# Kernel optimization log

Hardware: AMD Instinct MI355X
Metric: run time of the kernel (lower is better)

The kernel has to match this reference:

```python
import jax, jax.numpy as jnp
import numpy as np

B, S, V, H = 64, 512, 128, 1024
TEMP = 1.0


def _lstm_layer(x_seq, W_ih, W_hh, b_ih, b_hh):
    """x_seq: (S, B, D_in) -> (S, B, H). PyTorch gate order: i, f, g, o."""
    Hh = W_hh.shape[1]
    Bb = x_seq.shape[1]
    # precompute input projections for all timesteps: (S, B, 4H)
    xW = jnp.einsum('sbd,gd->sbg', x_seq, W_ih) + (b_ih + b_hh)

    def step(carry, xw_t):
        h, c = carry
        gates = xw_t + h @ W_hh.T  # (B, 4H)
        i, f, g, o = jnp.split(gates, 4, axis=-1)
        i = jax.nn.sigmoid(i)
        f = jax.nn.sigmoid(f)
        g = jnp.tanh(g)
        o = jax.nn.sigmoid(o)
        c = f * c + i * g
        h = o * jnp.tanh(c)
        return (h, c), h

    h0 = jnp.zeros((Bb, Hh), dtype=x_seq.dtype)
    c0 = jnp.zeros((Bb, Hh), dtype=x_seq.dtype)
    _, hs = jax.lax.scan(step, (h0, c0), xW)
    return hs  # (S, B, H)


def setup_inputs() -> dict:
    key = jax.random.key(0)
    ks = jax.random.split(key, 11)
    s = 1.0 / np.sqrt(H)
    u = lambda k, shape: jax.random.uniform(k, shape, jnp.float32, -s, s)
    return {
        'x': jax.random.normal(ks[0], (B, S, V), jnp.float32),
        'W_ih0': u(ks[1], (4 * H, V)),
        'W_hh0': u(ks[2], (4 * H, H)),
        'b_ih0': u(ks[3], (4 * H,)),
        'b_hh0': u(ks[4], (4 * H,)),
        'W_ih1': u(ks[5], (4 * H, H)),
        'W_hh1': u(ks[6], (4 * H, H)),
        'b_ih1': u(ks[7], (4 * H,)),
        'b_hh1': u(ks[8], (4 * H,)),
        'W_fc': u(ks[9], (V, H)),
        'b_fc': u(ks[10], (V,)),
    }


def reference(x, W_ih0, W_hh0, b_ih0, b_hh0, W_ih1, W_hh1, b_ih1, b_hh1, W_fc, b_fc):
    xs = jnp.transpose(x, (1, 0, 2))  # (S, B, V)
    h1 = _lstm_layer(xs, W_ih0, W_hh0, b_ih0, b_hh0)   # (S, B, H)
    h2 = _lstm_layer(h1, W_ih1, W_hh1, b_ih1, b_hh1)   # (S, B, H)
    logits = jnp.einsum('sbh,vh->sbv', h2, W_fc) + b_fc  # (S, B, V)
    out = jax.nn.log_softmax(logits * TEMP, axis=-1)
    return jnp.transpose(out, (1, 0, 2))  # (B, S, V)
```

## Files before the change

### kernel.cpp

```cpp
#include <hip/hip_runtime.h>
#include <hip/hip_bf16.h>
#include <math.h>


#define S_LEN 512
#define B_SZ  64
#define V_SZ  128
#define H_SZ  1024
#define BH    65536
#define RING  32
#define SLOT  66560
#define FSTR  16
#define INVP  20

typedef unsigned short u16;
typedef unsigned short u16x8 __attribute__((ext_vector_type(8)));
typedef __bf16         bf16x8 __attribute__((ext_vector_type(8)));
typedef float          f32x4  __attribute__((ext_vector_type(4)));
typedef int            i32x4  __attribute__((ext_vector_type(4)));

__device__ __forceinline__ u16 f2bf(float f) {
    unsigned int u = __float_as_uint(f);
    u += 0x7fffu + ((u >> 16) & 1u);
    return (u16)(u >> 16);
}
__device__ __forceinline__ f32x4 mfma16(u16x8 a, u16x8 b, f32x4 c) {
    return __builtin_amdgcn_mfma_f32_16x16x32_bf16(
        __builtin_bit_cast(bf16x8, a), __builtin_bit_cast(bf16x8, b), c, 0, 0, 0);
}
__device__ __forceinline__ f32x4 mfma16(i32x4 a, u16x8 b, f32x4 c) {
    return __builtin_amdgcn_mfma_f32_16x16x32_bf16(
        __builtin_bit_cast(bf16x8, a), __builtin_bit_cast(bf16x8, b), c, 0, 0, 0);
}

__device__ __forceinline__ void ld_g(i32x4& d, const u16* p) {
    asm volatile("global_load_dwordx4 %0, %1, off" : "=v"(d) : "v"(p));
}
__device__ __forceinline__ void st_coh16(u16* p, u16x8 v) {
    i32x4 vv = __builtin_bit_cast(i32x4, v);
    asm volatile("global_store_dwordx4 %0, %1, off sc0 sc1" :: "v"(p), "v"(vv));
}
__device__ __forceinline__ int ld_flag(const int* p) {
    int v;
    asm volatile("global_load_dword %0, %1, off sc0 sc1\n\ts_waitcnt vmcnt(0)"
                 : "=v"(v) : "v"(p) : "memory");
    return v;
}
__device__ __forceinline__ void st_flag(int* p, int v) {
    asm volatile("global_store_dword %0, %1, off sc0 sc1" :: "v"(p), "v"(v));
}
#define WAITV(n) asm volatile("s_waitcnt vmcnt(" #n ")" ::: "memory")
#define LGKM0    asm volatile("s_waitcnt lgkmcnt(0)" ::: "memory")
#define SCHEDB   __builtin_amdgcn_sched_barrier(0)

__device__ __forceinline__ void l2_acquire_inv() {
    __builtin_amdgcn_fence(__ATOMIC_ACQUIRE, "agent");
}

__global__ __launch_bounds__(256) void cvt_kernel(const float* __restrict__ s,
                                                  u16* __restrict__ d, int n)
{
    int i = (blockIdx.x * 256 + threadIdx.x) * 4;
    if (i >= n) return;
    float4 v = *(const float4*)(s + i);
    ushort4 o;
    o.x = f2bf(v.x); o.y = f2bf(v.y); o.z = f2bf(v.z); o.w = f2bf(v.w);
    *(ushort4*)(d + i) = o;
}

union SMemL {
    struct { u16 whh[64 * 1024]; u16 wih[64 * 128]; u16 tr[4][384]; } l0;
    struct { u16 w[64 * 1024]; u16 tr[4][384]; } l1;
    float lg[16][132];
};

__global__ __launch_bounds__(256, 1) void persist_kernel(
    const u16* __restrict__ xb,
    const u16* __restrict__ Wih0c, const u16* __restrict__ Whh0c,
    const u16* __restrict__ Wih1c, const u16* __restrict__ Whh1c,
    const u16* __restrict__ Wfcc,
    const float* __restrict__ bih0, const float* __restrict__ bhh0,
    const float* __restrict__ bih1, const float* __restrict__ bhh1,
    const float* __restrict__ bfc,
    u16* __restrict__ h0b, u16* __restrict__ h1b,
    int* __restrict__ flagL0, int* __restrict__ flagL1, int* __restrict__ flagFC,
    float* __restrict__ out)
{
    __shared__ SMemL sm;
    const int bid = blockIdx.x, tid = threadIdx.x;
    const int wave = tid >> 6, lane = tid & 63;
    const int l16 = lane & 15, kgi = lane >> 4, kg8 = kgi * 8;

    if (bid < 64) {
        const int j0 = bid * 16, jj = j0 + l16;
        for (int ch = tid; ch < 1024; ch += 256) {
            int row = ch >> 4, kc = ch & 15;
            int gr = (row >> 4) * H_SZ + j0 + (row & 15);
            int bo = (row * 256 + kc * 16) ^ ((row & 7) << 4);
            *(u16x8*)((char*)sm.l0.wih + bo) = *(const u16x8*)(Wih0c + (size_t)gr * V_SZ + kc * 8);
        }
        for (int ch = tid; ch < 8192; ch += 256) {
            int row = ch >> 7, kc = ch & 127;
            int gr = (row >> 4) * H_SZ + j0 + (row & 15);
            int bo = (row * 2048 + kc * 16) ^ ((row & 7) << 4);
            *(u16x8*)((char*)sm.l0.whh + bo) = *(const u16x8*)(Whh0c + (size_t)gr * H_SZ + kc * 8);
        }
        __syncthreads();

        const float bii = bih0[jj]            + bhh0[jj];
        const float bif = bih0[H_SZ + jj]     + bhh0[H_SZ + jj];
        const float big = bih0[2 * H_SZ + jj] + bhh0[2 * H_SZ + jj];
        const float bio = bih0[3 * H_SZ + jj] + bhh0[3 * H_SZ + jj];

        const int swz = (l16 & 7) << 4;
        int whh_rb[4], wih_rb[4];
        #pragma unroll
        for (int g = 0; g < 4; ++g) {
            whh_rb[g] = (g * 16 + l16) * 2048 + kgi * 16;
            wih_rb[g] = (g * 16 + l16) * 256 + kgi * 16;
        }
        const int arow = wave * 16 + l16;
        const u16* xrow = xb + (size_t)arow * (S_LEN * V_SZ);
        u16* trw = sm.l0.tr[wave];
        float creg[4] = {0.f, 0.f, 0.f, 0.f};

        for (int t = 0; t < S_LEN; ++t) {
            i32x4 xq[4];
            {
                const u16* xp = xrow + (size_t)t * V_SZ + kg8;
                #pragma unroll
                for (int i = 0; i < 4; ++i) ld_g(xq[i], xp + i * 32);
            }
            {
                const int* p = nullptr; int tgt = 0;
                if (tid < 64)                      { p = flagL0 + tid * FSTR;        tgt = t; }
                else if (tid < 192 && t >= RING)   { p = flagL1 + (tid - 64) * FSTR; tgt = t - (RING - 1); }
                if (p && tgt > 0) while (ld_flag(p) < tgt) __builtin_amdgcn_s_sleep(2);
                __syncthreads();
            }
            if (t >= INVP && (t % INVP) == 0) l2_acquire_inv();
            WAITV(0); SCHEDB;

            f32x4 acc[4][2] = {};
            auto ISSUE = [&](i32x4 (&buf)[8], const u16* base) {
                #pragma unroll
                for (int q = 0; q < 8; ++q) ld_g(buf[q], base + q * 32);
            };
            auto COMP = [&](i32x4 (&buf)[8], int k0) {
                #pragma unroll
                for (int q = 0; q < 8; ++q)
                    #pragma unroll
                    for (int g = 0; g < 4; ++g)
                        acc[g][q & 1] = mfma16(buf[q],
                            *(const u16x8*)((char*)sm.l0.whh + ((whh_rb[g] + (k0 + q) * 64) ^ swz)),
                            acc[g][q & 1]);
            };
            const u16* aB = h0b + (size_t)((t - 1) & (RING - 1)) * SLOT
                          + (size_t)arow * H_SZ + kg8;
            i32x4 b0[8], b1[8], b2[8];
            ISSUE(b0, aB); ISSUE(b1, aB + 256); ISSUE(b2, aB + 512);
            SCHEDB;
            #pragma unroll
            for (int i = 0; i < 4; ++i)
                #pragma unroll
                for (int g = 0; g < 4; ++g)
                    acc[g][i & 1] = mfma16(xq[i],
                        *(const u16x8*)((char*)sm.l0.wih + ((wih_rb[g] + i * 64) ^ swz)),
                        acc[g][i & 1]);
            WAITV(16); SCHEDB; COMP(b0, 0);  ISSUE(b0, aB + 768);
            WAITV(16); SCHEDB; COMP(b1, 8);
            WAITV(8);  SCHEDB; COMP(b2, 16);
            WAITV(0);  SCHEDB; COMP(b0, 24);

            {
                u16* hout = h0b + (size_t)(t & (RING - 1)) * SLOT;
                #pragma unroll
                for (int r = 0; r < 4; ++r) {
                    const float ip = acc[0][0][r] + acc[0][1][r] + bii;
                    const float fp = acc[1][0][r] + acc[1][1][r] + bif;
                    const float gp = acc[2][0][r] + acc[2][1][r] + big;
                    const float op = acc[3][0][r] + acc[3][1][r] + bio;
                    const float iv = 1.f / (1.f + expf(-ip));
                    const float fv = 1.f / (1.f + expf(-fp));
                    const float gv = tanhf(gp);
                    const float ov = 1.f / (1.f + expf(-op));
                    const float cv = fv * creg[r] + iv * gv;
                    creg[r] = cv;
                    trw[(kgi * 4 + r) * 24 + l16] = f2bf(ov * tanhf(cv));
                }
                LGKM0; SCHEDB;
                if (lane < 32) {
                    int m = lane >> 1, jb = lane & 1;
                    u16x8 v = *(const u16x8*)&trw[m * 24 + jb * 8];
                    st_coh16(hout + (size_t)(wave * 16 + m) * H_SZ + j0 + jb * 8, v);
                }
                WAITV(0);
            }
            __syncthreads();
            if (tid == 0) st_flag(flagL0 + bid * FSTR, t + 1);
        }
        return;
    }

    if (bid < 192) {
        const int lb = bid - 64, j0 = lb * 8, jj2 = j0 + (l16 & 7);
        for (int ch = tid; ch < 8192; ch += 256) {
            int ldsrow = ch >> 7, kc = ch & 127;
            int region = ldsrow >> 5, rl = ldsrow & 31;
            int gr = (rl >> 3) * H_SZ + j0 + (rl & 7);
            const u16* src = (region ? Whh1c : Wih1c) + (size_t)gr * H_SZ + kc * 8;
            int bo = (ldsrow * 2048 + kc * 16) ^ ((ldsrow & 7) << 4);
            *(u16x8*)((char*)sm.l1.w + bo) = *(const u16x8*)src;
        }
        __syncthreads();

        const float bii = bih1[jj2]            + bhh1[jj2];
        const float bif = bih1[H_SZ + jj2]     + bhh1[H_SZ + jj2];
        const float big = bih1[2 * H_SZ + jj2] + bhh1[2 * H_SZ + jj2];
        const float bio = bih1[3 * H_SZ + jj2] + bhh1[3 * H_SZ + jj2];
        const bool lo = (l16 < 8);

        const int swz = (l16 & 7) << 4;
        int wrb[2][2];
        #pragma unroll
        for (int region = 0; region < 2; ++region)
            #pragma unroll
            for (int nt = 0; nt < 2; ++nt)
                wrb[region][nt] = (region * 32 + nt * 16 + l16) * 2048 + kgi * 16;
        const int arow = wave * 16 + l16;
        u16* trw = sm.l1.tr[wave];
        float creg[4] = {0.f, 0.f, 0.f, 0.f};

        for (int t = 0; t < S_LEN; ++t) {
            {
                const int* p = nullptr; int tgt = 0;
                if (tid < 64)                        { p = flagL0 + tid * FSTR;         tgt = t + 1; }
                else if (tid < 192)                  { p = flagL1 + (tid - 64) * FSTR;  tgt = t; }
                else if (tid < 196 && t >= RING)     { p = flagFC + (tid - 192) * FSTR; tgt = t - (RING - 1); }
                if (p && tgt > 0) while (ld_flag(p) < tgt) __builtin_amdgcn_s_sleep(2);
                __syncthreads();
            }
            if (t >= INVP && (t % INVP) == 0) l2_acquire_inv();

            f32x4 acc[2][2] = {};
            auto ISSUE = [&](i32x4 (&buf)[8], const u16* base) {
                #pragma unroll
                for (int q = 0; q < 8; ++q) ld_g(buf[q], base + q * 32);
            };
            auto COMP = [&](i32x4 (&buf)[8], int region, int k0) {
                #pragma unroll
                for (int q = 0; q < 8; ++q)
                    #pragma unroll
                    for (int nt = 0; nt < 2; ++nt)
                        acc[nt][q & 1] = mfma16(buf[q],
                            *(const u16x8*)((char*)sm.l1.w + ((wrb[region][nt] + (k0 + q) * 64) ^ swz)),
                            acc[nt][q & 1]);
            };
            const u16* a1 = h0b + (size_t)(t & (RING - 1)) * SLOT + (size_t)arow * H_SZ + kg8;
            const u16* a2 = h1b + (size_t)((t - 1) & (RING - 1)) * SLOT + (size_t)arow * H_SZ + kg8;
            i32x4 b0[8], b1[8], b2[8];
            ISSUE(b0, a1); ISSUE(b1, a1 + 256); ISSUE(b2, a1 + 512);
            SCHEDB;
            WAITV(16); SCHEDB; COMP(b0, 0, 0);  ISSUE(b0, a1 + 768);
            WAITV(16); SCHEDB; COMP(b1, 0, 8);  ISSUE(b1, a2);
            WAITV(16); SCHEDB; COMP(b2, 0, 16); ISSUE(b2, a2 + 256);
            WAITV(16); SCHEDB; COMP(b0, 0, 24); ISSUE(b0, a2 + 512);
            WAITV(16); SCHEDB; COMP(b1, 1, 0);  ISSUE(b1, a2 + 768);
            WAITV(16); SCHEDB; COMP(b2, 1, 8);
            WAITV(8);  SCHEDB; COMP(b0, 1, 16);
            WAITV(0);  SCHEDB; COMP(b1, 1, 24);

            {
                #pragma unroll
                for (int r = 0; r < 4; ++r) {
                    const float s0 = acc[0][0][r] + acc[0][1][r];
                    const float s1 = acc[1][0][r] + acc[1][1][r];
                    const float q0 = __shfl_xor(s0, 8);
                    const float q1 = __shfl_xor(s1, 8);
                    const float ip = (lo ? s0 : q0) + bii;
                    const float fp = (lo ? q0 : s0) + bif;
                    const float gp = (lo ? s1 : q1) + big;
                    const float op = (lo ? q1 : s1) + bio;
                    const float iv = 1.f / (1.f + expf(-ip));
                    const float fv = 1.f / (1.f + expf(-fp));
                    const float gv = tanhf(gp);
                    const float ov = 1.f / (1.f + expf(-op));
                    const float cv = fv * creg[r] + iv * gv;
                    creg[r] = cv;
                    if (lo) trw[(kgi * 4 + r) * 24 + (l16 & 7)] = f2bf(ov * tanhf(cv));
                }
                LGKM0; SCHEDB;
                if (lane < 16) {
                    int m = lane;
                    u16x8 v = *(const u16x8*)&trw[m * 24];
                    st_coh16(h1b + (size_t)(t & (RING - 1)) * SLOT
                             + (size_t)(wave * 16 + m) * H_SZ + j0, v);
                }
                WAITV(0);
            }
            __syncthreads();
            if (tid == 0) st_flag(flagL1 + lb * FSTR, t + 1);
        }
        return;
    }

    {
        const int fb = bid - 192, m0 = fb * 16;
        const u16* wp[2];
        #pragma unroll
        for (int nt = 0; nt < 2; ++nt)
            wp[nt] = Wfcc + (size_t)(wave * 32 + nt * 16 + l16) * H_SZ + kg8;

        for (int t = 0; t < S_LEN; ++t) {
            {
                const int* p = nullptr; int tgt = 0;
                if (tid < 128) { p = flagL1 + tid * FSTR; tgt = t + 1; }
                if (p && tgt > 0) while (ld_flag(p) < tgt) __builtin_amdgcn_s_sleep(2);
                __syncthreads();
            }
            if (t >= INVP && (t % INVP) == 0) l2_acquire_inv();

            const u16* aB = h1b + (size_t)(t & (RING - 1)) * SLOT
                          + (size_t)(m0 + l16) * H_SZ + kg8;
            f32x4 acc[2][2] = {};
            i32x4 buf[8];
            WAITV(0);
            #pragma unroll
            for (int c = 0; c < 4; ++c) {
                #pragma unroll
                for (int q = 0; q < 8; ++q) ld_g(buf[q], aB + c * 256 + q * 32);
                WAITV(0); SCHEDB;
                #pragma unroll
                for (int q = 0; q < 8; ++q) {
                    #pragma unroll
                    for (int nt = 0; nt < 2; ++nt)
                        acc[nt][q & 1] = mfma16(buf[q],
                            *(const u16x8*)(wp[nt] + (c * 8 + q) * 32), acc[nt][q & 1]);
                }
            }
            #pragma unroll
            for (int nt = 0; nt < 2; ++nt)
                #pragma unroll
                for (int r = 0; r < 4; ++r) {
                    const int m = kgi * 4 + r, n = wave * 32 + nt * 16 + l16;
                    sm.lg[m][n] = acc[nt][0][r] + acc[nt][1][r] + bfc[n];
                }
            __syncthreads();
            const int row = tid >> 4, sub = tid & 15;
            float vals[8]; float mx = -1e30f;
            #pragma unroll
            for (int q = 0; q < 8; ++q) { vals[q] = sm.lg[row][sub * 8 + q]; mx = fmaxf(mx, vals[q]); }
            #pragma unroll
            for (int o = 1; o < 16; o <<= 1) mx = fmaxf(mx, __shfl_xor(mx, o));
            float se = 0.f;
            #pragma unroll
            for (int q = 0; q < 8; ++q) se += expf(vals[q] - mx);
            #pragma unroll
            for (int o = 1; o < 16; o <<= 1) se += __shfl_xor(se, o);
            const float ls = mx + logf(se);
            float* op = out + (size_t)(m0 + row) * (S_LEN * V_SZ) + (size_t)t * V_SZ + sub * 8;
            #pragma unroll
            for (int q = 0; q < 8; ++q) op[q] = vals[q] - ls;

            __syncthreads();
            if (tid == 0) st_flag(flagFC + fb * FSTR, t + 1);
        }
    }
}

extern "C" void kernel_launch(void* const* d_in, const int* in_sizes, int n_in,
                              void* d_out, int out_size, void* d_ws, size_t ws_size,
                              hipStream_t stream)
{
    const float* x    = (const float*)d_in[0];
    const float* Wih0 = (const float*)d_in[1];
    const float* Whh0 = (const float*)d_in[2];
    const float* bih0 = (const float*)d_in[3];
    const float* bhh0 = (const float*)d_in[4];
    const float* Wih1 = (const float*)d_in[5];
    const float* Whh1 = (const float*)d_in[6];
    const float* bih1 = (const float*)d_in[7];
    const float* bhh1 = (const float*)d_in[8];
    const float* Wfc  = (const float*)d_in[9];
    const float* bfc  = (const float*)d_in[10];
    float* out = (float*)d_out;

    u16* wih0 = (u16*)d_ws;
    u16* whh0 = wih0 + (size_t)4096 * 128;
    u16* wih1 = whh0 + (size_t)4096 * 1024;
    u16* whh1 = wih1 + (size_t)4096 * 1024;
    u16* wfc  = whh1 + (size_t)4096 * 1024;
    u16* xbuf = wfc  + (size_t)128 * 1024;
    u16* h0b  = xbuf + (size_t)B_SZ * S_LEN * V_SZ;
    u16* h1b  = h0b + (size_t)RING * SLOT;
    int* flags  = (int*)(h1b + (size_t)RING * SLOT);
    int* flagL0 = flags;
    int* flagL1 = flagL0 + 64 * FSTR;
    int* flagFC = flagL1 + 128 * FSTR;

    auto cvt = [&](const float* s, u16* d, int n) {
        cvt_kernel<<<(n / 4 + 255) / 256, 256, 0, stream>>>(s, d, n);
    };
    cvt(Wih0, wih0, 4096 * 128);
    cvt(Whh0, whh0, 4096 * 1024);
    cvt(Wih1, wih1, 4096 * 1024);
    cvt(Whh1, whh1, 4096 * 1024);
    cvt(Wfc,  wfc,  128 * 1024);
    cvt(x,    xbuf, B_SZ * S_LEN * V_SZ);
    hipMemsetAsync(h0b + (size_t)(RING - 1) * SLOT, 0, (size_t)BH * sizeof(u16), stream);
    hipMemsetAsync(h1b + (size_t)(RING - 1) * SLOT, 0, (size_t)BH * sizeof(u16), stream);
    hipMemsetAsync(flags, 0, (size_t)196 * FSTR * sizeof(int), stream);

    persist_kernel<<<196, 256, 0, stream>>>(
        xbuf, wih0, whh0, wih1, whh1, wfc,
        bih0, bhh0, bih1, bhh1, bfc,
        h0b, h1b, flagL0, flagL1, flagFC, out);
}
```

Before: 6.385 ms.

## Split layer-1 flag wait to overlap h0 GEMM, pad LDS rows instead of XOR swizzle

Layer-1 blocks now wait only on the layer-0 flag before starting the W_ih1·h0 half of the matmul. The layer-1 recurrent flag is polled asynchronously mid-computation and checked just before loading h1, so the wait on the slowest layer-1 block overlaps useful MFMA work. Flag polls use an async load with a single fast-path check before falling into the spin loop. Weight LDS tiles switch from XOR swizzle to padded row strides (1040/144), which simplifies addressing but uses more shared memory and adds an extra __syncthreads per step.

```diff
diff --git a/kernel.cpp b/kernel.cpp
--- a/kernel.cpp
+++ b/kernel.cpp
@@ -12,6 +12,7 @@
 #define SLOT  66560
 #define FSTR  16
 #define INVP  20
+#define WSTR  1040
 
 typedef unsigned short u16;
 typedef unsigned short u16x8 __attribute__((ext_vector_type(8)));
@@ -45,6 +46,12 @@
     asm volatile("global_load_dword %0, %1, off sc0 sc1\n\ts_waitcnt vmcnt(0)"
                  : "=v"(v) : "v"(p) : "memory");
     return v;
+}
+__device__ __forceinline__ void ld_flag_async(int& v, const int* p) {
+    asm volatile("global_load_dword %0, %1, off sc0 sc1" : "=v"(v) : "v"(p));
+}
+__device__ __forceinline__ void flag_fence(int& v) {
+    asm volatile("s_waitcnt vmcnt(0)" : "+v"(v) :: "memory");
 }
 __device__ __forceinline__ void st_flag(int* p, int v) {
     asm volatile("global_store_dword %0, %1, off sc0 sc1" :: "v"(p), "v"(v));
@@ -69,8 +76,8 @@
 }
 
 union SMemL {
-    struct { u16 whh[64 * 1024]; u16 wih[64 * 128]; u16 tr[4][384]; } l0;
-    struct { u16 w[64 * 1024]; u16 tr[4][384]; } l1;
+    struct { u16 whh[64 * WSTR]; u16 wih[64 * 144]; u16 tr[4][384]; } l0;
+    struct { u16 w[64 * WSTR]; u16 tr[4][384]; } l1;
     float lg[16][132];
 };
 
@@ -96,14 +103,14 @@
         for (int ch = tid; ch < 1024; ch += 256) {
             int row = ch >> 4, kc = ch & 15;
             int gr = (row >> 4) * H_SZ + j0 + (row & 15);
-            int bo = (row * 256 + kc * 16) ^ ((row & 7) << 4);
-            *(u16x8*)((char*)sm.l0.wih + bo) = *(const u16x8*)(Wih0c + (size_t)gr * V_SZ + kc * 8);
+            *(u16x8*)&sm.l0.wih[row * 144 + kc * 8] =
+                *(const u16x8*)(Wih0c + (size_t)gr * V_SZ + kc * 8);
         }
         for (int ch = tid; ch < 8192; ch += 256) {
             int row = ch >> 7, kc = ch & 127;
             int gr = (row >> 4) * H_SZ + j0 + (row & 15);
-            int bo = (row * 2048 + kc * 16) ^ ((row & 7) << 4);
-            *(u16x8*)((char*)sm.l0.whh + bo) = *(const u16x8*)(Whh0c + (size_t)gr * H_SZ + kc * 8);
+            *(u16x8*)&sm.l0.whh[row * WSTR + kc * 8] =
+                *(const u16x8*)(Whh0c + (size_t)gr * H_SZ + kc * 8);
         }
         __syncthreads();
 
@@ -112,12 +119,11 @@
         const float big = bih0[2 * H_SZ + jj] + bhh0[2 * H_SZ + jj];
         const float bio = bih0[3 * H_SZ + jj] + bhh0[3 * H_SZ + jj];
 
-        const int swz = (l16 & 7) << 4;
-        int whh_rb[4], wih_rb[4];
+        int whh_b[4], wih_b[4];
         #pragma unroll
         for (int g = 0; g < 4; ++g) {
-            whh_rb[g] = (g * 16 + l16) * 2048 + kgi * 16;
-            wih_rb[g] = (g * 16 + l16) * 256 + kgi * 16;
+            whh_b[g] = (g * 16 + l16) * WSTR + kg8;
+            wih_b[g] = (g * 16 + l16) * 144 + kg8;
         }
         const int arow = wave * 16 + l16;
         const u16* xrow = xb + (size_t)arow * (S_LEN * V_SZ);
@@ -131,15 +137,15 @@
                 #pragma unroll
                 for (int i = 0; i < 4; ++i) ld_g(xq[i], xp + i * 32);
             }
-            {
-                const int* p = nullptr; int tgt = 0;
-                if (tid < 64)                      { p = flagL0 + tid * FSTR;        tgt = t; }
-                else if (tid < 192 && t >= RING)   { p = flagL1 + (tid - 64) * FSTR; tgt = t - (RING - 1); }
-                if (p && tgt > 0) while (ld_flag(p) < tgt) __builtin_amdgcn_s_sleep(2);
-                __syncthreads();
-            }
+            const int* pA = nullptr; int tgtA = 0; int fvA = 0x7fffffff;
+            if (tid < 64)                    { pA = flagL0 + tid * FSTR;        tgtA = t; }
+            else if (tid < 192 && t >= RING) { pA = flagL1 + (tid - 64) * FSTR; tgtA = t - (RING - 1); }
+            if (pA && tgtA > 0) ld_flag_async(fvA, pA);
+            flag_fence(fvA);
+            if (pA && tgtA > 0 && fvA < tgtA)
+                while (ld_flag(pA) < tgtA) __builtin_amdgcn_s_sleep(2);
+            __syncthreads();
             if (t >= INVP && (t % INVP) == 0) l2_acquire_inv();
-            WAITV(0); SCHEDB;
 
             f32x4 acc[4][2] = {};
             auto ISSUE = [&](i32x4 (&buf)[8], const u16* base) {
@@ -152,7 +158,7 @@
                     #pragma unroll
                     for (int g = 0; g < 4; ++g)
                         acc[g][q & 1] = mfma16(buf[q],
-                            *(const u16x8*)((char*)sm.l0.whh + ((whh_rb[g] + (k0 + q) * 64) ^ swz)),
+                            *(const u16x8*)&sm.l0.whh[whh_b[g] + (k0 + q) * 32],
                             acc[g][q & 1]);
             };
             const u16* aB = h0b + (size_t)((t - 1) & (RING - 1)) * SLOT
@@ -165,8 +171,7 @@
                 #pragma unroll
                 for (int g = 0; g < 4; ++g)
                     acc[g][i & 1] = mfma16(xq[i],
-                        *(const u16x8*)((char*)sm.l0.wih + ((wih_rb[g] + i * 64) ^ swz)),
-                        acc[g][i & 1]);
+                        *(const u16x8*)&sm.l0.wih[wih_b[g] + i * 32], acc[g][i & 1]);
             WAITV(16); SCHEDB; COMP(b0, 0);  ISSUE(b0, aB + 768);
             WAITV(16); SCHEDB; COMP(b1, 8);
             WAITV(8);  SCHEDB; COMP(b2, 16);
@@ -209,8 +214,7 @@
             int region = ldsrow >> 5, rl = ldsrow & 31;
             int gr = (rl >> 3) * H_SZ + j0 + (rl & 7);
             const u16* src = (region ? Whh1c : Wih1c) + (size_t)gr * H_SZ + kc * 8;
-            int bo = (ldsrow * 2048 + kc * 16) ^ ((ldsrow & 7) << 4);
-            *(u16x8*)((char*)sm.l1.w + bo) = *(const u16x8*)src;
+            *(u16x8*)&sm.l1.w[ldsrow * WSTR + kc * 8] = *(const u16x8*)src;
         }
         __syncthreads();
 
@@ -220,26 +224,27 @@
         const float bio = bih1[3 * H_SZ + jj2] + bhh1[3 * H_SZ + jj2];
         const bool lo = (l16 < 8);
 
-        const int swz = (l16 & 7) << 4;
         int wrb[2][2];
         #pragma unroll
         for (int region = 0; region < 2; ++region)
             #pragma unroll
             for (int nt = 0; nt < 2; ++nt)
-                wrb[region][nt] = (region * 32 + nt * 16 + l16) * 2048 + kgi * 16;
+                wrb[region][nt] = (region * 32 + nt * 16 + l16) * WSTR + kg8;
         const int arow = wave * 16 + l16;
         u16* trw = sm.l1.tr[wave];
         float creg[4] = {0.f, 0.f, 0.f, 0.f};
 
         for (int t = 0; t < S_LEN; ++t) {
-            {
-                const int* p = nullptr; int tgt = 0;
-                if (tid < 64)                        { p = flagL0 + tid * FSTR;         tgt = t + 1; }
-                else if (tid < 192)                  { p = flagL1 + (tid - 64) * FSTR;  tgt = t; }
-                else if (tid < 196 && t >= RING)     { p = flagFC + (tid - 192) * FSTR; tgt = t - (RING - 1); }
-                if (p && tgt > 0) while (ld_flag(p) < tgt) __builtin_amdgcn_s_sleep(2);
-                __syncthreads();
-            }
+            const int* pA = nullptr; int tgtA = 0; int fvA = 0x7fffffff;
+            if (tid < 64)                               { pA = flagL0 + tid * FSTR;         tgtA = t + 1; }
+            else if (tid >= 192 && tid < 196 && t >= RING) { pA = flagFC + (tid - 192) * FSTR; tgtA = t - (RING - 1); }
+            const int* pB = (tid < 128 && t > 0) ? (flagL1 + tid * FSTR) : nullptr;
+            int fvB = 0x7fffffff;
+            if (pA && tgtA > 0) ld_flag_async(fvA, pA);
+            flag_fence(fvA);
+            if (pA && tgtA > 0 && fvA < tgtA)
+                while (ld_flag(pA) < tgtA) __builtin_amdgcn_s_sleep(2);
+            __syncthreads();
             if (t >= INVP && (t % INVP) == 0) l2_acquire_inv();
 
             f32x4 acc[2][2] = {};
@@ -253,22 +258,27 @@
                     #pragma unroll
                     for (int nt = 0; nt < 2; ++nt)
                         acc[nt][q & 1] = mfma16(buf[q],
-                            *(const u16x8*)((char*)sm.l1.w + ((wrb[region][nt] + (k0 + q) * 64) ^ swz)),
+                            *(const u16x8*)&sm.l1.w[wrb[region][nt] + (k0 + q) * 32],
                             acc[nt][q & 1]);
             };
             const u16* a1 = h0b + (size_t)(t & (RING - 1)) * SLOT + (size_t)arow * H_SZ + kg8;
             const u16* a2 = h1b + (size_t)((t - 1) & (RING - 1)) * SLOT + (size_t)arow * H_SZ + kg8;
             i32x4 b0[8], b1[8], b2[8];
             ISSUE(b0, a1); ISSUE(b1, a1 + 256); ISSUE(b2, a1 + 512);
-            SCHEDB;
             WAITV(16); SCHEDB; COMP(b0, 0, 0);  ISSUE(b0, a1 + 768);
-            WAITV(16); SCHEDB; COMP(b1, 0, 8);  ISSUE(b1, a2);
-            WAITV(16); SCHEDB; COMP(b2, 0, 16); ISSUE(b2, a2 + 256);
-            WAITV(16); SCHEDB; COMP(b0, 0, 24); ISSUE(b0, a2 + 512);
-            WAITV(16); SCHEDB; COMP(b1, 1, 0);  ISSUE(b1, a2 + 768);
-            WAITV(16); SCHEDB; COMP(b2, 1, 8);
-            WAITV(8);  SCHEDB; COMP(b0, 1, 16);
-            WAITV(0);  SCHEDB; COMP(b1, 1, 24);
+            WAITV(16); SCHEDB; COMP(b1, 0, 8);
+            WAITV(8);  SCHEDB; COMP(b2, 0, 16);
+            if (pB) ld_flag_async(fvB, pB);
+            WAITV(0);  SCHEDB; COMP(b0, 0, 24);
+            flag_fence(fvB);
+            if (pB && fvB < t)
+                while (ld_flag(pB) < t) __builtin_amdgcn_s_sleep(2);
+            __syncthreads();
+            ISSUE(b0, a2); ISSUE(b1, a2 + 256); ISSUE(b2, a2 + 512);
+            WAITV(16); SCHEDB; COMP(b0, 1, 0);  ISSUE(b0, a2 + 768);
+            WAITV(16); SCHEDB; COMP(b1, 1, 8);
+            WAITV(8);  SCHEDB; COMP(b2, 1, 16);
+            WAITV(0);  SCHEDB; COMP(b0, 1, 24);
 
             {
                 #pragma unroll
@@ -313,9 +323,12 @@
 
         for (int t = 0; t < S_LEN; ++t) {
             {
-                const int* p = nullptr; int tgt = 0;
-                if (tid < 128) { p = flagL1 + tid * FSTR; tgt = t + 1; }
-                if (p && tgt > 0) while (ld_flag(p) < tgt) __builtin_amdgcn_s_sleep(2);
+                const int* pA = (tid < 128) ? (flagL1 + tid * FSTR) : nullptr;
+                int fvA = 0x7fffffff;
+                if (pA) ld_flag_async(fvA, pA);
+                flag_fence(fvA);
+                if (pA && fvA < t + 1)
+                    while (ld_flag(pA) < t + 1) __builtin_amdgcn_s_sleep(2);
                 __syncthreads();
             }
             if (t >= INVP && (t % INVP) == 0) l2_acquire_inv();
```

New measurement: 6.629 ms. +3.8%, slower.

## Replace per-block flags with per-step atomic counters and coherent h loads

Applied to the files above, without the earlier changes.

Each block used to publish its own progress flag, and a whole wavefront polled every producer flag. Now each block atomically increments a per-timestep counter in a ring, and a single thread waits for the expected count. Loads of the hidden state bypass the caches (sc0 sc1), which replaces the periodic L2 acquire invalidation. The LDS weight layout also drops the XOR swizzle in favour of a padded row stride, trading extra LDS for simpler address math. Risks include atomic contention on each counter and possible LDS bank conflicts from the padded layout.

```diff
diff --git a/kernel.cpp b/kernel.cpp
--- a/kernel.cpp
+++ b/kernel.cpp
@@ -11,7 +11,7 @@
 #define RING  32
 #define SLOT  66560
 #define FSTR  16
-#define INVP  20
+#define WSTR  1040
 
 typedef unsigned short u16;
 typedef unsigned short u16x8 __attribute__((ext_vector_type(8)));
@@ -33,7 +33,10 @@
         __builtin_bit_cast(bf16x8, a), __builtin_bit_cast(bf16x8, b), c, 0, 0, 0);
 }
 
-__device__ __forceinline__ void ld_g(i32x4& d, const u16* p) {
+__device__ __forceinline__ void ld_cv(i32x4& d, const u16* p) {
+    asm volatile("global_load_dwordx4 %0, %1, off sc0 sc1" : "=v"(d) : "v"(p));
+}
+__device__ __forceinline__ void ld_ca(i32x4& d, const u16* p) {
     asm volatile("global_load_dwordx4 %0, %1, off" : "=v"(d) : "v"(p));
 }
 __device__ __forceinline__ void st_coh16(u16* p, u16x8 v) {
@@ -46,16 +49,12 @@
                  : "=v"(v) : "v"(p) : "memory");
     return v;
 }
-__device__ __forceinline__ void st_flag(int* p, int v) {
-    asm volatile("global_store_dword %0, %1, off sc0 sc1" :: "v"(p), "v"(v));
+__device__ __forceinline__ void wait_ge(const int* p, int tgt) {
+    while (ld_flag(p) < tgt) __builtin_amdgcn_s_sleep(8);
 }
 #define WAITV(n) asm volatile("s_waitcnt vmcnt(" #n ")" ::: "memory")
 #define LGKM0    asm volatile("s_waitcnt lgkmcnt(0)" ::: "memory")
 #define SCHEDB   __builtin_amdgcn_sched_barrier(0)
-
-__device__ __forceinline__ void l2_acquire_inv() {
-    __builtin_amdgcn_fence(__ATOMIC_ACQUIRE, "agent");
-}
 
 __global__ __launch_bounds__(256) void cvt_kernel(const float* __restrict__ s,
                                                   u16* __restrict__ d, int n)
@@ -69,8 +68,8 @@
 }
 
 union SMemL {
-    struct { u16 whh[64 * 1024]; u16 wih[64 * 128]; u16 tr[4][384]; } l0;
-    struct { u16 w[64 * 1024]; u16 tr[4][384]; } l1;
+    struct { u16 whh[64 * WSTR]; u16 wih[64 * 144]; u16 tr[4][384]; } l0;
+    struct { u16 w[64 * WSTR]; u16 tr[4][384]; } l1;
     float lg[16][132];
 };
 
@@ -83,7 +82,7 @@
     const float* __restrict__ bih1, const float* __restrict__ bhh1,
     const float* __restrict__ bfc,
     u16* __restrict__ h0b, u16* __restrict__ h1b,
-    int* __restrict__ flagL0, int* __restrict__ flagL1, int* __restrict__ flagFC,
+    int* __restrict__ cntL0, int* __restrict__ cntL1, int* __restrict__ cntFC,
     float* __restrict__ out)
 {
     __shared__ SMemL sm;
@@ -96,14 +95,14 @@
         for (int ch = tid; ch < 1024; ch += 256) {
             int row = ch >> 4, kc = ch & 15;
             int gr = (row >> 4) * H_SZ + j0 + (row & 15);
-            int bo = (row * 256 + kc * 16) ^ ((row & 7) << 4);
-            *(u16x8*)((char*)sm.l0.wih + bo) = *(const u16x8*)(Wih0c + (size_t)gr * V_SZ + kc * 8);
+            *(u16x8*)&sm.l0.wih[row * 144 + kc * 8] =
+                *(const u16x8*)(Wih0c + (size_t)gr * V_SZ + kc * 8);
         }
         for (int ch = tid; ch < 8192; ch += 256) {
             int row = ch >> 7, kc = ch & 127;
             int gr = (row >> 4) * H_SZ + j0 + (row & 15);
-            int bo = (row * 2048 + kc * 16) ^ ((row & 7) << 4);
-            *(u16x8*)((char*)sm.l0.whh + bo) = *(const u16x8*)(Whh0c + (size_t)gr * H_SZ + kc * 8);
+            *(u16x8*)&sm.l0.whh[row * WSTR + kc * 8] =
+                *(const u16x8*)(Whh0c + (size_t)gr * H_SZ + kc * 8);
         }
         __syncthreads();
 
@@ -112,12 +111,11 @@
         const float big = bih0[2 * H_SZ + jj] + bhh0[2 * H_SZ + jj];
         const float bio = bih0[3 * H_SZ + jj] + bhh0[3 * H_SZ + jj];
 
-        const int swz = (l16 & 7) << 4;
-        int whh_rb[4], wih_rb[4];
+        int whh_b[4], wih_b[4];
         #pragma unroll
         for (int g = 0; g < 4; ++g) {
-            whh_rb[g] = (g * 16 + l16) * 2048 + kgi * 16;
-            wih_rb[g] = (g * 16 + l16) * 256 + kgi * 16;
+            whh_b[g] = (g * 16 + l16) * WSTR + kg8;
+            wih_b[g] = (g * 16 + l16) * 144 + kg8;
         }
         const int arow = wave * 16 + l16;
         const u16* xrow = xb + (size_t)arow * (S_LEN * V_SZ);
@@ -129,22 +127,19 @@
             {
                 const u16* xp = xrow + (size_t)t * V_SZ + kg8;
                 #pragma unroll
-                for (int i = 0; i < 4; ++i) ld_g(xq[i], xp + i * 32);
+                for (int i = 0; i < 4; ++i) ld_ca(xq[i], xp + i * 32);
             }
-            {
-                const int* p = nullptr; int tgt = 0;
-                if (tid < 64)                      { p = flagL0 + tid * FSTR;        tgt = t; }
-                else if (tid < 192 && t >= RING)   { p = flagL1 + (tid - 64) * FSTR; tgt = t - (RING - 1); }
-                if (p && tgt > 0) while (ld_flag(p) < tgt) __builtin_amdgcn_s_sleep(2);
-                __syncthreads();
-            }
-            if (t >= INVP && (t % INVP) == 0) l2_acquire_inv();
+            if (tid == 0 && t >= 1)
+                wait_ge(cntL0 + ((t - 1) & 31) * FSTR, 64 * (((t - 1) >> 5) + 1));
+            if (tid == 64 && t >= RING)
+                wait_ge(cntL1 + (t & 31) * FSTR, 128 * (t >> 5));
+            __syncthreads();
             WAITV(0); SCHEDB;
 
             f32x4 acc[4][2] = {};
             auto ISSUE = [&](i32x4 (&buf)[8], const u16* base) {
                 #pragma unroll
-                for (int q = 0; q < 8; ++q) ld_g(buf[q], base + q * 32);
+                for (int q = 0; q < 8; ++q) ld_cv(buf[q], base + q * 32);
             };
             auto COMP = [&](i32x4 (&buf)[8], int k0) {
                 #pragma unroll
@@ -152,7 +147,7 @@
                     #pragma unroll
                     for (int g = 0; g < 4; ++g)
                         acc[g][q & 1] = mfma16(buf[q],
-                            *(const u16x8*)((char*)sm.l0.whh + ((whh_rb[g] + (k0 + q) * 64) ^ swz)),
+                            *(const u16x8*)&sm.l0.whh[whh_b[g] + (k0 + q) * 32],
                             acc[g][q & 1]);
             };
             const u16* aB = h0b + (size_t)((t - 1) & (RING - 1)) * SLOT
@@ -165,8 +160,7 @@
                 #pragma unroll
                 for (int g = 0; g < 4; ++g)
                     acc[g][i & 1] = mfma16(xq[i],
-                        *(const u16x8*)((char*)sm.l0.wih + ((wih_rb[g] + i * 64) ^ swz)),
-                        acc[g][i & 1]);
+                        *(const u16x8*)&sm.l0.wih[wih_b[g] + i * 32], acc[g][i & 1]);
             WAITV(16); SCHEDB; COMP(b0, 0);  ISSUE(b0, aB + 768);
             WAITV(16); SCHEDB; COMP(b1, 8);
             WAITV(8);  SCHEDB; COMP(b2, 16);
@@ -197,7 +191,7 @@
                 WAITV(0);
             }
             __syncthreads();
-            if (tid == 0) st_flag(flagL0 + bid * FSTR, t + 1);
+            if (tid == 0) atomicAdd(cntL0 + (t & 31) * FSTR, 1);
         }
         return;
     }
@@ -209,8 +203,7 @@
             int region = ldsrow >> 5, rl = ldsrow & 31;
             int gr = (rl >> 3) * H_SZ + j0 + (rl & 7);
             const u16* src = (region ? Whh1c : Wih1c) + (size_t)gr * H_SZ + kc * 8;
-            int bo = (ldsrow * 2048 + kc * 16) ^ ((ldsrow & 7) << 4);
-            *(u16x8*)((char*)sm.l1.w + bo) = *(const u16x8*)src;
+            *(u16x8*)&sm.l1.w[ldsrow * WSTR + kc * 8] = *(const u16x8*)src;
         }
         __syncthreads();
 
@@ -220,32 +213,29 @@
         const float bio = bih1[3 * H_SZ + jj2] + bhh1[3 * H_SZ + jj2];
         const bool lo = (l16 < 8);
 
-        const int swz = (l16 & 7) << 4;
         int wrb[2][2];
         #pragma unroll
         for (int region = 0; region < 2; ++region)
             #pragma unroll
             for (int nt = 0; nt < 2; ++nt)
-                wrb[region][nt] = (region * 32 + nt * 16 + l16) * 2048 + kgi * 16;
+                wrb[region][nt] = (region * 32 + nt * 16 + l16) * WSTR + kg8;
         const int arow = wave * 16 + l16;
         u16* trw = sm.l1.tr[wave];
         float creg[4] = {0.f, 0.f, 0.f, 0.f};
 
         for (int t = 0; t < S_LEN; ++t) {
-            {
-                const int* p = nullptr; int tgt = 0;
-                if (tid < 64)                        { p = flagL0 + tid * FSTR;         tgt = t + 1; }
-                else if (tid < 192)                  { p = flagL1 + (tid - 64) * FSTR;  tgt = t; }
-                else if (tid < 196 && t >= RING)     { p = flagFC + (tid - 192) * FSTR; tgt = t - (RING - 1); }
-                if (p && tgt > 0) while (ld_flag(p) < tgt) __builtin_amdgcn_s_sleep(2);
-                __syncthreads();
-            }
-            if (t >= INVP && (t % INVP) == 0) l2_acquire_inv();
+            if (tid == 0)
+                wait_ge(cntL0 + (t & 31) * FSTR, 64 * ((t >> 5) + 1));
+            if (tid == 64 && t >= 1)
+                wait_ge(cntL1 + ((t - 1) & 31) * FSTR, 128 * (((t - 1) >> 5) + 1));
+            if (tid == 128 && t >= RING)
+                wait_ge(cntFC + (t & 31) * FSTR, 4 * (t >> 5));
+            __syncthreads();
 
             f32x4 acc[2][2] = {};
             auto ISSUE = [&](i32x4 (&buf)[8], const u16* base) {
                 #pragma unroll
-                for (int q = 0; q < 8; ++q) ld_g(buf[q], base + q * 32);
+                for (int q = 0; q < 8; ++q) ld_cv(buf[q], base + q * 32);
             };
             auto COMP = [&](i32x4 (&buf)[8], int region, int k0) {
                 #pragma unroll
@@ -253,7 +243,7 @@
                     #pragma unroll
                     for (int nt = 0; nt < 2; ++nt)
                         acc[nt][q & 1] = mfma16(buf[q],
-                            *(const u16x8*)((char*)sm.l1.w + ((wrb[region][nt] + (k0 + q) * 64) ^ swz)),
+                            *(const u16x8*)&sm.l1.w[wrb[region][nt] + (k0 + q) * 32],
                             acc[nt][q & 1]);
             };
             const u16* a1 = h0b + (size_t)(t & (RING - 1)) * SLOT + (size_t)arow * H_SZ + kg8;
@@ -299,7 +289,7 @@
                 WAITV(0);
             }
             __syncthreads();
-            if (tid == 0) st_flag(flagL1 + lb * FSTR, t + 1);
+            if (tid == 0) atomicAdd(cntL1 + (t & 31) * FSTR, 1);
         }
         return;
     }
@@ -312,23 +302,18 @@
             wp[nt] = Wfcc + (size_t)(wave * 32 + nt * 16 + l16) * H_SZ + kg8;
 
         for (int t = 0; t < S_LEN; ++t) {
-            {
-                const int* p = nullptr; int tgt = 0;
-                if (tid < 128) { p = flagL1 + tid * FSTR; tgt = t + 1; }
-                if (p && tgt > 0) while (ld_flag(p) < tgt) __builtin_amdgcn_s_sleep(2);
-                __syncthreads();
-            }
-            if (t >= INVP && (t % INVP) == 0) l2_acquire_inv();
+            if (tid == 0)
+                wait_ge(cntL1 + (t & 31) * FSTR, 128 * ((t >> 5) + 1));
+            __syncthreads();
 
             const u16* aB = h1b + (size_t)(t & (RING - 1)) * SLOT
                           + (size_t)(m0 + l16) * H_SZ + kg8;
             f32x4 acc[2][2] = {};
             i32x4 buf[8];
-            WAITV(0);
             #pragma unroll
             for (int c = 0; c < 4; ++c) {
                 #pragma unroll
-                for (int q = 0; q < 8; ++q) ld_g(buf[q], aB + c * 256 + q * 32);
+                for (int q = 0; q < 8; ++q) ld_cv(buf[q], aB + c * 256 + q * 32);
                 WAITV(0); SCHEDB;
                 #pragma unroll
                 for (int q = 0; q < 8; ++q) {
@@ -363,7 +348,7 @@
             for (int q = 0; q < 8; ++q) op[q] = vals[q] - ls;
 
             __syncthreads();
-            if (tid == 0) st_flag(flagFC + fb * FSTR, t + 1);
+            if (tid == 0) atomicAdd(cntFC + (t & 31) * FSTR, 1);
         }
     }
 }
@@ -393,10 +378,10 @@
     u16* xbuf = wfc  + (size_t)128 * 1024;
     u16* h0b  = xbuf + (size_t)B_SZ * S_LEN * V_SZ;
     u16* h1b  = h0b + (size_t)RING * SLOT;
-    int* flags  = (int*)(h1b + (size_t)RING * SLOT);
-    int* flagL0 = flags;
-    int* flagL1 = flagL0 + 64 * FSTR;
-    int* flagFC = flagL1 + 128 * FSTR;
+    int* cnts  = (int*)(h1b + (size_t)RING * SLOT);
+    int* cntL0 = cnts;
+    int* cntL1 = cntL0 + RING * FSTR;
+    int* cntFC = cntL1 + RING * FSTR;
 
     auto cvt = [&](const float* s, u16* d, int n) {
         cvt_kernel<<<(n / 4 + 255) / 256, 256, 0, stream>>>(s, d, n);
@@ -409,10 +394,10 @@
     cvt(x,    xbuf, B_SZ * S_LEN * V_SZ);
     hipMemsetAsync(h0b + (size_t)(RING - 1) * SLOT, 0, (size_t)BH * sizeof(u16), stream);
     hipMemsetAsync(h1b + (size_t)(RING - 1) * SLOT, 0, (size_t)BH * sizeof(u16), stream);
-    hipMemsetAsync(flags, 0, (size_t)196 * FSTR * sizeof(int), stream);
+    hipMemsetAsync(cnts, 0, (size_t)3 * RING * FSTR * sizeof(int), stream);
 
     persist_kernel<<<196, 256, 0, stream>>>(
         xbuf, wih0, whh0, wih1, whh1, wfc,
         bih0, bhh0, bih1, bhh1, bfc,
-        h0b, h1b, flagL0, flagL1, flagFC, out);
-}
+        h0b, h1b, cntL0, cntL1, cntFC, out);
+}
```

After: 7.386 ms. +15.7%, slower.
